# Kernel optimization log

Measured on AMD Instinct MI355X. Metric: run time of the kernel, lower is better.

Reference implementation:

```python
import jax, jax.numpy as jnp
import numpy as np


def _perm_mats():
    E = np.zeros((36, 9), np.float32)
    D = np.zeros((9, 36), np.float32)
    c = 0
    for i in range(8):
        for j in range(i + 1, 9):
            E[c, i] = 1.0
            E[c, j] = 1.0
            D[i, c] = 1.0
            D[j, c] = 1.0
            c += 1
    assert c == 36
    return E, D


def setup_inputs() -> dict:
    key = jax.random.key(0)
    B = 32768
    # binary candidate mask: [B, 9 digits, 9 rows, 9 cols]
    mask = jnp.round(jax.random.uniform(key, (B, 9, 9, 9), dtype=jnp.float32))
    E, D = _perm_mats()
    return {"mask": mask, "enc": jnp.asarray(E), "dec": jnp.asarray(D)}


def _nn_compare(x, v):
    # NNCompare: triangular bump == 1 exactly when x == v (for integer-valued x)
    return jnp.minimum(jax.nn.relu(x - (v - 1.0)), jax.nn.relu((v + 1.0) - x))


def _nn_and(x, y):
    return jnp.clip(jnp.minimum(x, y), 0.0, 1.0)


def reference(mask, enc, dec):
    B = mask.shape[0]
    # encode_permutations: 1x1 conv 9 -> 36 (pair selection)
    perms = jnp.einsum('oc,bchw->bohw', enc, mask)          # [B,36,9,9]
    perms = _nn_compare(perms, 2.0)                          # cell contains exactly this pair
    # sum_all_permutations: 1x1 conv 36 -> 1, then == 1
    sum_p = _nn_compare(jnp.sum(perms, axis=1, keepdims=True), 1.0)  # [B,1,9,9]
    perms = _nn_and(perms, sum_p)                            # broadcast over 36 channels
    # box downsample: grouped 3x3 stride-3 sum conv
    down = perms.reshape(B, 36, 3, 3, 3, 3).sum(axis=(3, 5))  # [B,36,3,3]
    down = _nn_compare(down, 2.0)                              # exactly two such cells in box
    up = jnp.repeat(jnp.repeat(down, 3, axis=2), 3, axis=3)    # [B,36,9,9]
    up = _nn_and(up, 1.0 - perms)                              # other cells in the box
    # decode_permutations: 1x1 conv 36 -> 9
    erase = jnp.einsum('oc,bchw->bohw', dec, up)               # [B,9,9,9]
    return _nn_and(mask, 1.0 - erase)
```

## Files before the change

kernel.cpp:

```cpp
#include <hip/hip_runtime.h>
#include <stdint.h>


__global__ __launch_bounds__(256) void sudoku_box_kernel(
    const float* __restrict__ mask, float* __restrict__ out) {
  const int t = blockIdx.x * 256 + threadIdx.x;
  const int board = t / 9;
  const int bi = t - board * 9;
  const int base = board * 729 + (bi / 3) * 27 + (bi % 3) * 3;

  const float* p = mask + base;
  float v[9][3][3];
#pragma unroll
  for (int d = 0; d < 9; ++d)
#pragma unroll
    for (int r = 0; r < 3; ++r)
#pragma unroll
      for (int c = 0; c < 3; ++c)
        v[d][r][c] = p[d * 81 + r * 9 + c];

  uint32_t cellm[9] = {0, 0, 0, 0, 0, 0, 0, 0, 0};
#pragma unroll
  for (int d = 0; d < 9; ++d)
#pragma unroll
    for (int r = 0; r < 3; ++r)
#pragma unroll
      for (int c = 0; c < 3; ++c)
        cellm[r * 3 + c] |= (v[d][r][c] != 0.0f ? 1u : 0u) << d;

  uint32_t pairm[9];
#pragma unroll
  for (int j = 0; j < 9; ++j)
    pairm[j] = (__popc(cellm[j]) == 2) ? cellm[j] : 0u;

  bool naked[9];
#pragma unroll
  for (int j = 0; j < 9; ++j) {
    int cnt = 0;
#pragma unroll
    for (int k = 0; k < 9; ++k) cnt += (pairm[k] == pairm[j]);
    naked[j] = (pairm[j] != 0u) && (cnt == 2);
  }

  uint32_t fin[9];
#pragma unroll
  for (int j = 0; j < 9; ++j) {
    uint32_t er = 0;
#pragma unroll
    for (int k = 0; k < 9; ++k)
      if (naked[k] && pairm[k] != pairm[j]) er |= pairm[k];
    fin[j] = cellm[j] & ~er;
  }

  float* q = out + base;
#pragma unroll
  for (int d = 0; d < 9; ++d)
#pragma unroll
    for (int r = 0; r < 3; ++r)
#pragma unroll
      for (int c = 0; c < 3; ++c)
        q[d * 81 + r * 9 + c] = (float)((fin[r * 3 + c] >> d) & 1u);
}

extern "C" void kernel_launch(void* const* d_in, const int* in_sizes, int n_in,
                              void* d_out, int out_size, void* d_ws, size_t ws_size,
                              hipStream_t stream) {
  const float* mask = (const float*)d_in[0];
  float* out = (float*)d_out;
  const int B = in_sizes[0] / 729;
  const int nbox = B * 9;
  const int grid = nbox / 256;
  sudoku_box_kernel<<<grid, 256, 0, stream>>>(mask, out);
}
```

Baseline: 179.7 us.

## Split into compress, box-logic and expand kernels with coalesced vector I/O

Replaces the single kernel, whose per-thread strided scalar loads and stores were poorly coalesced, with three kernels. The first packs the float mask into a bitset using float4 loads, the second runs the naked-pair box logic on that bitset and writes 16-bit per-cell masks, and the third expands those masks back to floats with float4 stores. This is meant to make the large float reads and writes fully coalesced, at the cost of two extra launches and a small intermediate round trip through the workspace. Sizes are hardcoded to the test batch.

```diff
diff --git a/kernel.cpp b/kernel.cpp
--- a/kernel.cpp
+++ b/kernel.cpp
@@ -2,31 +2,49 @@
 #include <stdint.h>
 
 
-__global__ __launch_bounds__(256) void sudoku_box_kernel(
-    const float* __restrict__ mask, float* __restrict__ out) {
+#define NFLOAT 23887872
+#define NBYTE  2985984
+#define NBOX   294912
+#define NVEC4  5971968
+
+__global__ __launch_bounds__(256) void k1_compress(
+    const float* __restrict__ in, uint8_t* __restrict__ bits) {
+  const int t = blockIdx.x * 256 + threadIdx.x;
+  const float4* in4 = (const float4*)in;
+  float4 a = in4[2 * t];
+  float4 b = in4[2 * t + 1];
+  uint32_t w = (a.x != 0.0f ? 1u : 0u)
+             | (a.y != 0.0f ? 2u : 0u)
+             | (a.z != 0.0f ? 4u : 0u)
+             | (a.w != 0.0f ? 8u : 0u)
+             | (b.x != 0.0f ? 16u : 0u)
+             | (b.y != 0.0f ? 32u : 0u)
+             | (b.z != 0.0f ? 64u : 0u)
+             | (b.w != 0.0f ? 128u : 0u);
+  bits[t] = (uint8_t)w;
+}
+
+__global__ __launch_bounds__(256) void k2_boxlogic(
+    const uint32_t* __restrict__ bw, unsigned short* __restrict__ fin) {
   const int t = blockIdx.x * 256 + threadIdx.x;
   const int board = t / 9;
   const int bi = t - board * 9;
-  const int base = board * 729 + (bi / 3) * 27 + (bi % 3) * 3;
-
-  const float* p = mask + base;
-  float v[9][3][3];
-#pragma unroll
-  for (int d = 0; d < 9; ++d)
-#pragma unroll
-    for (int r = 0; r < 3; ++r)
-#pragma unroll
-      for (int c = 0; c < 3; ++c)
-        v[d][r][c] = p[d * 81 + r * 9 + c];
+  const int bo = (bi / 3) * 27 + (bi % 3) * 3;
+  const int S = board * 729;
 
   uint32_t cellm[9] = {0, 0, 0, 0, 0, 0, 0, 0, 0};
 #pragma unroll
   for (int d = 0; d < 9; ++d)
 #pragma unroll
-    for (int r = 0; r < 3; ++r)
-#pragma unroll
-      for (int c = 0; c < 3; ++c)
-        cellm[r * 3 + c] |= (v[d][r][c] != 0.0f ? 1u : 0u) << d;
+    for (int r = 0; r < 3; ++r) {
+      const int f = S + d * 81 + bo + r * 9;
+      const int idx = f >> 5, sh = f & 31;
+      const uint64_t v = (uint64_t)bw[idx] | ((uint64_t)bw[idx + 1] << 32);
+      const uint32_t b3 = (uint32_t)(v >> sh) & 7u;
+      cellm[r * 3 + 0] |= (b3 & 1u) << d;
+      cellm[r * 3 + 1] |= ((b3 >> 1) & 1u) << d;
+      cellm[r * 3 + 2] |= ((b3 >> 2) & 1u) << d;
+    }
 
   uint32_t pairm[9];
 #pragma unroll
@@ -42,24 +60,34 @@
     naked[j] = (pairm[j] != 0u) && (cnt == 2);
   }
 
-  uint32_t fin[9];
+  unsigned short* fb = fin + board * 81;
 #pragma unroll
   for (int j = 0; j < 9; ++j) {
     uint32_t er = 0;
 #pragma unroll
     for (int k = 0; k < 9; ++k)
       if (naked[k] && pairm[k] != pairm[j]) er |= pairm[k];
-    fin[j] = cellm[j] & ~er;
+    const int cell = bo + (j / 3) * 9 + (j % 3);
+    fb[cell] = (unsigned short)(cellm[j] & ~er);
   }
+}
 
-  float* q = out + base;
+__global__ __launch_bounds__(256) void k3_expand(
+    const unsigned short* __restrict__ fin, float* __restrict__ out) {
+  const int t = blockIdx.x * 256 + threadIdx.x;
+  const int e0 = t * 4;
+  float4 v;
+  float* vp = &v.x;
 #pragma unroll
-  for (int d = 0; d < 9; ++d)
-#pragma unroll
-    for (int r = 0; r < 3; ++r)
-#pragma unroll
-      for (int c = 0; c < 3; ++c)
-        q[d * 81 + r * 9 + c] = (float)((fin[r * 3 + c] >> d) & 1u);
+  for (int q = 0; q < 4; ++q) {
+    const int e = e0 + q;
+    const int b = e / 729;
+    const int rem = e - b * 729;
+    const int d = rem / 81;
+    const int cell = rem - d * 81;
+    vp[q] = (float)((fin[b * 81 + cell] >> d) & 1u);
+  }
+  ((float4*)out)[t] = v;
 }
 
 extern "C" void kernel_launch(void* const* d_in, const int* in_sizes, int n_in,
@@ -67,8 +95,10 @@
                               hipStream_t stream) {
   const float* mask = (const float*)d_in[0];
   float* out = (float*)d_out;
-  const int B = in_sizes[0] / 729;
-  const int nbox = B * 9;
-  const int grid = nbox / 256;
-  sudoku_box_kernel<<<grid, 256, 0, stream>>>(mask, out);
+  uint8_t* bits = (uint8_t*)d_ws;
+  unsigned short* fin = (unsigned short*)((uint8_t*)d_ws + NBYTE);
+
+  k1_compress<<<NBYTE / 256, 256, 0, stream>>>(mask, bits);
+  k2_boxlogic<<<NBOX / 256, 256, 0, stream>>>((const uint32_t*)bits, fin);
+  k3_expand<<<NVEC4 / 256, 256, 0, stream>>>(fin, out);
 }
```

Result: slower. 183.9 us (+2.3%).
